# Kernel tuning notes

Hardware: AMD Instinct MI355X
Metric: run time of the kernel (lower is better)

The kernel has to match this reference:

```python
import jax, jax.numpy as jnp
import numpy as np

D_IN = 4096
D_OUT = 4096
RANK = 16
ALPHA = 32
SCALE = ALPHA / RANK


def setup_inputs() -> dict:
    key = jax.random.key(0)
    k_x, k_w, k_b, k_a = jax.random.split(key, 4)
    x = jax.random.normal(k_x, (4, 2048, D_IN), dtype=jnp.float32)
    weight = jax.random.normal(k_w, (D_OUT, D_IN), dtype=jnp.float32) * (1.0 / np.sqrt(D_IN))
    bias = jax.random.normal(k_b, (D_OUT,), dtype=jnp.float32)
    lora_A = jax.random.normal(k_a, (RANK, D_IN), dtype=jnp.float32) * 0.01
    lora_B = jnp.zeros((D_OUT, RANK), dtype=jnp.float32)
    return {"x": x, "weight": weight, "bias": bias, "lora_A": lora_A, "lora_B": lora_B}


def reference(x, weight, bias, lora_A, lora_B):
    # base linear: y = x @ W^T + b   -> [B, S, D_OUT]
    orig_out = jnp.einsum("bsd,od->bso", x, weight) + bias
    # low-rank path: (x @ A^T) @ B^T * (alpha/rank)
    lora_out = jnp.einsum("bsr,or->bso", jnp.einsum("bsd,rd->bsr", x, lora_A), lora_B)
    return orig_out + lora_out * SCALE
```

## Files before the change

### kernel.cpp

```cpp
#include <hip/hip_runtime.h>
#include <stdint.h>

#define DIN   4096
#define DOUT  4096
#define RANK  16
#define MTOT  8192
#define LSCALE 2.0f

typedef unsigned short u16;
typedef __bf16 bf16x8 __attribute__((ext_vector_type(8)));
typedef float  f32x4  __attribute__((ext_vector_type(4)));
typedef u16    u16x8  __attribute__((ext_vector_type(8)));

__device__ __forceinline__ u16 f2bf(float f) {
    uint32_t u = __builtin_bit_cast(uint32_t, f);
    u = (u + 0x7FFFu + ((u >> 16) & 1u)) >> 16;
    return (u16)u;
}

__device__ __forceinline__ u16x8 pack8(f32x4 a, f32x4 b) {
    u16x8 o;
    o[0] = f2bf(a[0]); o[1] = f2bf(a[1]); o[2] = f2bf(a[2]); o[3] = f2bf(a[3]);
    o[4] = f2bf(b[0]); o[5] = f2bf(b[1]); o[6] = f2bf(b[2]); o[7] = f2bf(b[3]);
    return o;
}

#define GLDS16(g, l) __builtin_amdgcn_global_load_lds( \
    (const __attribute__((address_space(1))) void*)(g), \
    (__attribute__((address_space(3))) void*)(l), 16, 0, 0)

__global__ __launch_bounds__(256) void k_convert_x(const float* __restrict__ x,
                                                   u16* __restrict__ xb) {
    long i = ((long)blockIdx.x * 256 + threadIdx.x) * 8;
    f32x4 a = *(const f32x4*)(x + i);
    f32x4 b = *(const f32x4*)(x + i + 4);
    *(u16x8*)(xb + i) = pack8(a, b);
}

__global__ __launch_bounds__(256) void k_build_weff(const float* __restrict__ W,
                                                    const float* __restrict__ A,
                                                    const float* __restrict__ B,
                                                    u16* __restrict__ wb) {
    long t = (long)blockIdx.x * 256 + threadIdx.x;
    long i = t * 8;
    int o = (int)(i >> 12);
    int d = (int)(i & (DIN - 1));
    float sB[RANK];
#pragma unroll
    for (int r = 0; r < RANK; ++r) sB[r] = B[o * RANK + r] * LSCALE;
    f32x4 w0 = *(const f32x4*)(W + i);
    f32x4 w1 = *(const f32x4*)(W + i + 4);
#pragma unroll
    for (int r = 0; r < RANK; ++r) {
        f32x4 a0 = *(const f32x4*)(A + (long)r * DIN + d);
        f32x4 a1 = *(const f32x4*)(A + (long)r * DIN + d + 4);
        w0 += a0 * sB[r];
        w1 += a1 * sB[r];
    }
    *(u16x8*)(wb + i) = pack8(w0, w1);
}

#define BM 256
#define BN 256
#define BK 64
#define NT (DIN / BK)

#define MFMA16(d, a, b) d = __builtin_amdgcn_mfma_f32_16x16x32_bf16(a, b, d, 0, 0, 0)
#define ABAR()   asm volatile("s_barrier" ::: "memory")
#define GATE8()  asm volatile("s_waitcnt vmcnt(8)" ::: "memory")
#define GATE10() asm volatile("s_waitcnt vmcnt(10)" ::: "memory")
#define PRIO1() __builtin_amdgcn_s_setprio(1)
#define PRIO0() __builtin_amdgcn_s_setprio(0)

#define QUADK(mo, no, AF, BF) \
    _Pragma("unroll") \
    for (int kk = 0; kk < 2; ++kk) { \
        _Pragma("unroll") \
        for (int m = 0; m < 4; ++m) { \
            _Pragma("unroll") \
            for (int n = 0; n < 2; ++n) { \
                MFMA16(acc[(mo)+m][(no)+n], AF[m][kk], BF[n][kk]); \
            } \
        } \
    }

#define READ_A4(DST, P, RB) \
    _Pragma("unroll") \
    for (int m = 0; m < 4; ++m) { \
        DST[m][0] = *(const bf16x8*)((P) + (RB) + m*1024 + go0); \
        DST[m][1] = *(const bf16x8*)((P) + (RB) + m*1024 + go1); \
    }
#define READ_B2(DST, P, RB) \
    _Pragma("unroll") \
    for (int n = 0; n < 2; ++n) { \
        DST[n][0] = *(const bf16x8*)((P) + (RB) + n*1024 + go0); \
        DST[n][1] = *(const bf16x8*)((P) + (RB) + n*1024 + go1); \
    }

__global__ __launch_bounds__(512, 2) void k_gemm_ws(const u16* __restrict__ xb,
                                                    const u16* __restrict__ wb,
                                                    const float* __restrict__ bias,
                                                    float* __restrict__ out) {
    constexpr int K = DIN, N = DOUT;
    __shared__ alignas(16) u16 lds[65536];

    const int nchunk = gridDim.x >> 3;
    const int bid = blockIdx.x;
    const int wg  = (bid & 7) * nchunk + (bid >> 3);
    const int bm  = (wg & 31) * BM;
    const int bn  = (wg >> 5) * BN;

    const int tid  = threadIdx.x;
    const int lane = tid & 63;
    const int wid  = tid >> 6;
    const int wr   = wid >> 2;
    const int wc   = wid & 3;
    const int lrow = lane & 15;
    const int kgrp = lane >> 4;

    const int srow = tid >> 3;
    const int sgl  = (tid & 7) ^ (srow & 7);
    const u16* const aSrcB = xb + (long)(bm + srow) * K + sgl * 8;
    const u16* const bSrcB = wb + (long)(bn + srow) * K + sgl * 8;

#define STAGE_A(c, buf, kt) GLDS16(aSrcB + (long)(64*(c))*K + (kt)*BK, \
                                   lds + (buf)*16384 + (c)*4096 + tid*8)
#define STAGE_B(c, buf, kt) GLDS16(bSrcB + (long)(64*(c))*K + (kt)*BK, \
                                   lds + 32768 + (buf)*16384 + (c)*4096 + tid*8)

    const int go0 = (kgrp ^ (lrow & 7)) * 8;
    const int go1 = go0 ^ 32;
    const int arL = (wr*64 + lrow) * 64;
    const int arH = arL + 128*64;
    const int brL = (wc*32 + lrow) * 64;
    const int brH = brL + 128*64;

    const u16* const pA0 = lds;
    const u16* const pA1 = lds + 16384;
    const u16* const pB0 = lds + 32768;
    const u16* const pB1 = lds + 49152;

    f32x4 acc[8][4];
#pragma unroll
    for (int m = 0; m < 8; ++m)
#pragma unroll
        for (int n = 0; n < 4; ++n) acc[m][n] = (f32x4){0.f, 0.f, 0.f, 0.f};

    bf16x8 afL[4][2], afH[4][2], bfB[2][2], bfAe[2][2], bfAo[2][2];

    STAGE_A(0, 0, 0); STAGE_A(1, 0, 0);
    STAGE_B(0, 0, 0); STAGE_B(1, 0, 0);
    STAGE_B(2, 0, 0); STAGE_B(3, 0, 0);
    STAGE_A(2, 0, 0); STAGE_A(3, 0, 0);
    STAGE_A(0, 1, 1); STAGE_A(1, 1, 1);
    STAGE_B(0, 1, 1); STAGE_B(1, 1, 1);
    STAGE_B(2, 1, 1); STAGE_B(3, 1, 1);
    GATE10();
    ABAR();
    READ_A4(afL, pA0, arL);
    READ_B2(bfAe, pB0, brL);

    for (int it = 0; it < NT/2; ++it) {
        const int t   = 2*it;
        const int kt1 = t + 1;
        const int kt2 = (t + 2) & (NT - 1);
        const int kt3 = (t + 3) & (NT - 1);

        GATE8(); ABAR();
        STAGE_A(2, 1, kt1); STAGE_A(3, 1, kt1);
        READ_B2(bfB, pB0, brH);
        PRIO1(); QUADK(0, 0, afL, bfAe); PRIO0();

        GATE8(); ABAR();
        STAGE_A(0, 0, kt2); STAGE_A(1, 0, kt2);
        READ_A4(afH, pA0, arH);
        PRIO1(); QUADK(0, 2, afL, bfB); PRIO0();

        ABAR();
        STAGE_B(0, 0, kt2); STAGE_B(1, 0, kt2);
        STAGE_B(2, 0, kt2); STAGE_B(3, 0, kt2);
        PRIO1(); QUADK(4, 2, afH, bfB); PRIO0();

        GATE10(); ABAR();
        READ_A4(afL, pA1, arL);
        READ_B2(bfAo, pB1, brL);
        PRIO1(); QUADK(4, 0, afH, bfAe); PRIO0();

        GATE8(); ABAR();
        STAGE_A(2, 0, kt2); STAGE_A(3, 0, kt2);
        READ_B2(bfB, pB1, brH);
        PRIO1(); QUADK(0, 0, afL, bfAo); PRIO0();

        GATE8(); ABAR();
        STAGE_A(0, 1, kt3); STAGE_A(1, 1, kt3);
        READ_A4(afH, pA1, arH);
        PRIO1(); QUADK(0, 2, afL, bfB); PRIO0();

        ABAR();
        STAGE_B(0, 1, kt3); STAGE_B(1, 1, kt3);
        STAGE_B(2, 1, kt3); STAGE_B(3, 1, kt3);
        PRIO1(); QUADK(4, 2, afH, bfB); PRIO0();

        GATE10(); ABAR();
        READ_A4(afL, pA0, arL);
        READ_B2(bfAe, pB0, brL);
        PRIO1(); QUADK(4, 0, afH, bfAo); PRIO0();
    }
    asm volatile("s_waitcnt vmcnt(0)" ::: "memory");

    const int orow = bm + wr*64 + kgrp*4;
    const int ocol = bn + wc*32 + lrow;
#pragma unroll
    for (int n = 0; n < 4; ++n) {
        const int col = ocol + (n & 1)*16 + (n >> 1)*128;
        const float bj = bias[col];
#pragma unroll
        for (int m = 0; m < 8; ++m) {
            const int row = orow + (m & 3)*16 + (m >> 2)*128;
#pragma unroll
            for (int r = 0; r < 4; ++r)
                out[(long)(row + r) * N + col] = acc[m][n][r] + bj;
        }
    }
}

__global__ __launch_bounds__(64) void k_lora_T(const float* __restrict__ x,
                                               const float* __restrict__ A,
                                               float* __restrict__ T) {
    const int m = blockIdx.x;
    const int lane = threadIdx.x;
    const float* xr = x + (long)m * DIN;
    float acc[RANK];
#pragma unroll
    for (int r = 0; r < RANK; ++r) acc[r] = 0.f;
    for (int k = lane * 4; k < DIN; k += 64 * 4) {
        f32x4 xv = *(const f32x4*)(xr + k);
#pragma unroll
        for (int r = 0; r < RANK; ++r) {
            f32x4 av = *(const f32x4*)(A + (long)r * DIN + k);
            acc[r] += xv[0] * av[0] + xv[1] * av[1] + xv[2] * av[2] + xv[3] * av[3];
        }
    }
#pragma unroll
    for (int r = 0; r < RANK; ++r)
        for (int off = 32; off > 0; off >>= 1) acc[r] += __shfl_down(acc[r], off);
    if (lane == 0) {
#pragma unroll
        for (int r = 0; r < RANK; ++r) T[(long)m * RANK + r] = acc[r] * LSCALE;
    }
}

__global__ __launch_bounds__(256) void k_gemm_nows(const float* __restrict__ x,
                                                   const float* __restrict__ W,
                                                   const float* __restrict__ bias,
                                                   const float* __restrict__ T,
                                                   const float* __restrict__ lB,
                                                   float* __restrict__ out) {
    constexpr int FBM = 128, FBN = 128, FBK = 32, K = DIN, N = DOUT;
    __shared__ __align__(16) u16 As[FBM * FBK];
    __shared__ __align__(16) u16 Bs[FBN * FBK];

    const int tid = threadIdx.x;
    const int bm = blockIdx.y * FBM;
    const int bn = blockIdx.x * FBN;
    const int lane = tid & 63;
    const int wid  = tid >> 6;
    const int wr = wid >> 1, wc = wid & 1;
    const int lrow = lane & 15;
    const int kgrp = lane >> 4;

    const int c0 = tid, c1 = tid + 256;
    const float* aS0 = x + (long)(bm + (c0 >> 2)) * K + (c0 & 3) * 8;
    const float* aS1 = x + (long)(bm + (c1 >> 2)) * K + (c1 & 3) * 8;
    const float* bS0 = W + (long)(bn + (c0 >> 2)) * K + (c0 & 3) * 8;
    const float* bS1 = W + (long)(bn + (c1 >> 2)) * K + (c1 & 3) * 8;
    u16* aD0 = As + c0 * 8;  u16* aD1 = As + c1 * 8;
    u16* bD0 = Bs + c0 * 8;  u16* bD1 = Bs + c1 * 8;

    const u16* aR = As + (wr * 64 + lrow) * FBK + kgrp * 8;
    const u16* bR = Bs + (wc * 64 + lrow) * FBK + kgrp * 8;

    f32x4 acc[4][4];
#pragma unroll
    for (int i = 0; i < 4; ++i)
#pragma unroll
        for (int j = 0; j < 4; ++j) acc[i][j] = (f32x4){0.f, 0.f, 0.f, 0.f};

    for (int k0 = 0; k0 < K; k0 += FBK) {
        f32x4 a00 = *(const f32x4*)aS0, a01 = *(const f32x4*)(aS0 + 4);
        f32x4 a10 = *(const f32x4*)aS1, a11 = *(const f32x4*)(aS1 + 4);
        f32x4 b00 = *(const f32x4*)bS0, b01 = *(const f32x4*)(bS0 + 4);
        f32x4 b10 = *(const f32x4*)bS1, b11 = *(const f32x4*)(bS1 + 4);
        aS0 += FBK; aS1 += FBK; bS0 += FBK; bS1 += FBK;
        if (k0) __syncthreads();
        *(u16x8*)aD0 = pack8(a00, a01);
        *(u16x8*)aD1 = pack8(a10, a11);
        *(u16x8*)bD0 = pack8(b00, b01);
        *(u16x8*)bD1 = pack8(b10, b11);
        __syncthreads();

        bf16x8 af[4], bf[4];
#pragma unroll
        for (int i = 0; i < 4; ++i) af[i] = *(const bf16x8*)(aR + i * 16 * FBK);
#pragma unroll
        for (int j = 0; j < 4; ++j) bf[j] = *(const bf16x8*)(bR + j * 16 * FBK);
#pragma unroll
        for (int i = 0; i < 4; ++i)
#pragma unroll
            for (int j = 0; j < 4; ++j)
                acc[i][j] = __builtin_amdgcn_mfma_f32_16x16x32_bf16(af[i], bf[j], acc[i][j], 0, 0, 0);
    }

#pragma unroll
    for (int j = 0; j < 4; ++j) {
        const int col = bn + wc * 64 + j * 16 + lrow;
        const float bj = bias[col];
        float bl[RANK];
#pragma unroll
        for (int q = 0; q < RANK; ++q) bl[q] = lB[(long)col * RANK + q];
#pragma unroll
        for (int i = 0; i < 4; ++i) {
            const int row0 = bm + wr * 64 + i * 16 + kgrp * 4;
#pragma unroll
            for (int r = 0; r < 4; ++r) {
                const int row = row0 + r;
                const float* Trow = T + (long)row * RANK;
                float s = bj;
#pragma unroll
                for (int q = 0; q < RANK; ++q) s += Trow[q] * bl[q];
                out[(long)row * N + col] = acc[i][j][r] + s;
            }
        }
    }
}

extern "C" void kernel_launch(void* const* d_in, const int* in_sizes, int n_in,
                              void* d_out, int out_size, void* d_ws, size_t ws_size,
                              hipStream_t stream) {
    const float* x    = (const float*)d_in[0];
    const float* W    = (const float*)d_in[1];
    const float* bias = (const float*)d_in[2];
    const float* lA   = (const float*)d_in[3];
    const float* lB   = (const float*)d_in[4];
    float* out = (float*)d_out;

    const size_t xb_bytes = (size_t)MTOT * DIN * sizeof(u16);
    const size_t wb_bytes = (size_t)DOUT * DIN * sizeof(u16);

    if (ws_size >= xb_bytes + wb_bytes) {
        u16* xb = (u16*)d_ws;
        u16* wb = (u16*)((char*)d_ws + xb_bytes);
        k_convert_x <<<(int)((long)MTOT * DIN / 8 / 256), 256, 0, stream>>>(x, xb);
        k_build_weff<<<(int)((long)DOUT * DIN / 8 / 256), 256, 0, stream>>>(W, lA, lB, wb);
        k_gemm_ws   <<<(MTOT / BM) * (DOUT / BN), 512, 0, stream>>>(xb, wb, bias, out);
    } else {
        float* T = (float*)d_ws;
        k_lora_T   <<<MTOT, 64, 0, stream>>>(x, lA, T);
        k_gemm_nows<<<dim3(DOUT / 128, MTOT / 128), 256, 0, stream>>>(x, W, bias, T, lB, out);
    }
}
```

Before: 332.2 us.

## Restructure GEMM main loop into single-tile four-phase pipeline with contiguous warp tiles

```diff
diff --git a/kernel.cpp b/kernel.cpp
--- a/kernel.cpp
+++ b/kernel.cpp
@@ -67,10 +67,11 @@
 
 #define MFMA16(d, a, b) d = __builtin_amdgcn_mfma_f32_16x16x32_bf16(a, b, d, 0, 0, 0)
 #define ABAR()   asm volatile("s_barrier" ::: "memory")
-#define GATE8()  asm volatile("s_waitcnt vmcnt(8)" ::: "memory")
-#define GATE10() asm volatile("s_waitcnt vmcnt(10)" ::: "memory")
-#define PRIO1() __builtin_amdgcn_s_setprio(1)
-#define PRIO0() __builtin_amdgcn_s_setprio(0)
+#define LGKM0()  asm volatile("s_waitcnt lgkmcnt(0)" ::: "memory")
+#define GATE4()  asm volatile("s_waitcnt vmcnt(4)" ::: "memory")
+#define SBAR0()  __builtin_amdgcn_sched_barrier(0)
+#define PRIO1()  __builtin_amdgcn_s_setprio(1)
+#define PRIO0()  __builtin_amdgcn_s_setprio(0)
 
 #define QUADK(mo, no, AF, BF) \
     _Pragma("unroll") \
@@ -84,19 +85,6 @@
         } \
     }
 
-#define READ_A4(DST, P, RB) \
-    _Pragma("unroll") \
-    for (int m = 0; m < 4; ++m) { \
-        DST[m][0] = *(const bf16x8*)((P) + (RB) + m*1024 + go0); \
-        DST[m][1] = *(const bf16x8*)((P) + (RB) + m*1024 + go1); \
-    }
-#define READ_B2(DST, P, RB) \
-    _Pragma("unroll") \
-    for (int n = 0; n < 2; ++n) { \
-        DST[n][0] = *(const bf16x8*)((P) + (RB) + n*1024 + go0); \
-        DST[n][1] = *(const bf16x8*)((P) + (RB) + n*1024 + go1); \
-    }
-
 __global__ __launch_bounds__(512, 2) void k_gemm_ws(const u16* __restrict__ xb,
                                                     const u16* __restrict__ wb,
                                                     const float* __restrict__ bias,
@@ -130,15 +118,8 @@
 
     const int go0 = (kgrp ^ (lrow & 7)) * 8;
     const int go1 = go0 ^ 32;
-    const int arL = (wr*64 + lrow) * 64;
-    const int arH = arL + 128*64;
-    const int brL = (wc*32 + lrow) * 64;
-    const int brH = brL + 128*64;
-
-    const u16* const pA0 = lds;
-    const u16* const pA1 = lds + 16384;
-    const u16* const pB0 = lds + 32768;
-    const u16* const pB1 = lds + 49152;
+    const int arow = (wr*128 + lrow) * 64;
+    const int brow = (wc*64  + lrow) * 64;
 
     f32x4 acc[8][4];
 #pragma unroll
@@ -146,77 +127,84 @@
 #pragma unroll
         for (int n = 0; n < 4; ++n) acc[m][n] = (f32x4){0.f, 0.f, 0.f, 0.f};
 
-    bf16x8 afL[4][2], afH[4][2], bfB[2][2], bfAe[2][2], bfAo[2][2];
+    bf16x8 af[4][2], bfLo[2][2], bfHi[2][2];
 
     STAGE_A(0, 0, 0); STAGE_A(1, 0, 0);
+    STAGE_A(2, 0, 0); STAGE_A(3, 0, 0);
     STAGE_B(0, 0, 0); STAGE_B(1, 0, 0);
     STAGE_B(2, 0, 0); STAGE_B(3, 0, 0);
-    STAGE_A(2, 0, 0); STAGE_A(3, 0, 0);
-    STAGE_A(0, 1, 1); STAGE_A(1, 1, 1);
     STAGE_B(0, 1, 1); STAGE_B(1, 1, 1);
     STAGE_B(2, 1, 1); STAGE_B(3, 1, 1);
-    GATE10();
-    ABAR();
-    READ_A4(afL, pA0, arL);
-    READ_B2(bfAe, pB0, brL);
-
-    for (int it = 0; it < NT/2; ++it) {
-        const int t   = 2*it;
-        const int kt1 = t + 1;
+    GATE4();
+    __syncthreads();
+
+    for (int t = 0; t < NT; ++t) {
+        const int cur = t & 1, nxt = cur ^ 1;
+        const int kt1 = (t + 1) & (NT - 1);
         const int kt2 = (t + 2) & (NT - 1);
-        const int kt3 = (t + 3) & (NT - 1);
-
-        GATE8(); ABAR();
-        STAGE_A(2, 1, kt1); STAGE_A(3, 1, kt1);
-        READ_B2(bfB, pB0, brH);
-        PRIO1(); QUADK(0, 0, afL, bfAe); PRIO0();
-
-        GATE8(); ABAR();
-        STAGE_A(0, 0, kt2); STAGE_A(1, 0, kt2);
-        READ_A4(afH, pA0, arH);
-        PRIO1(); QUADK(0, 2, afL, bfB); PRIO0();
-
-        ABAR();
-        STAGE_B(0, 0, kt2); STAGE_B(1, 0, kt2);
-        STAGE_B(2, 0, kt2); STAGE_B(3, 0, kt2);
-        PRIO1(); QUADK(4, 2, afH, bfB); PRIO0();
-
-        GATE10(); ABAR();
-        READ_A4(afL, pA1, arL);
-        READ_B2(bfAo, pB1, brL);
-        PRIO1(); QUADK(4, 0, afH, bfAe); PRIO0();
-
-        GATE8(); ABAR();
-        STAGE_A(2, 0, kt2); STAGE_A(3, 0, kt2);
-        READ_B2(bfB, pB1, brH);
-        PRIO1(); QUADK(0, 0, afL, bfAo); PRIO0();
-
-        GATE8(); ABAR();
-        STAGE_A(0, 1, kt3); STAGE_A(1, 1, kt3);
-        READ_A4(afH, pA1, arH);
-        PRIO1(); QUADK(0, 2, afL, bfB); PRIO0();
-
-        ABAR();
-        STAGE_B(0, 1, kt3); STAGE_B(1, 1, kt3);
-        STAGE_B(2, 1, kt3); STAGE_B(3, 1, kt3);
-        PRIO1(); QUADK(4, 2, afH, bfB); PRIO0();
-
-        GATE10(); ABAR();
-        READ_A4(afL, pA0, arL);
-        READ_B2(bfAe, pB0, brL);
-        PRIO1(); QUADK(4, 0, afH, bfAo); PRIO0();
+        const u16* const cA = lds + cur * 16384;
+        const u16* const cB = lds + 32768 + cur * 16384;
+
+#pragma unroll
+        for (int mf = 0; mf < 4; ++mf) {
+            const u16* b = cA + arow + mf * 1024;
+            af[mf][0] = *(const bf16x8*)(b + go0);
+            af[mf][1] = *(const bf16x8*)(b + go1);
+        }
+#pragma unroll
+        for (int nf = 0; nf < 2; ++nf) {
+            const u16* b = cB + brow + nf * 1024;
+            bfLo[nf][0] = *(const bf16x8*)(b + go0);
+            bfLo[nf][1] = *(const bf16x8*)(b + go1);
+        }
+        STAGE_A(0, nxt, kt1); STAGE_A(1, nxt, kt1);
+        ABAR();
+        LGKM0(); SBAR0();
+        PRIO1(); QUADK(0, 0, af, bfLo); PRIO0(); SBAR0();
+        ABAR();
+
+#pragma unroll
+        for (int nf = 0; nf < 2; ++nf) {
+            const u16* b = cB + brow + (nf + 2) * 1024;
+            bfHi[nf][0] = *(const bf16x8*)(b + go0);
+            bfHi[nf][1] = *(const bf16x8*)(b + go1);
+        }
+        STAGE_A(2, nxt, kt1); STAGE_A(3, nxt, kt1);
+        ABAR();
+        LGKM0(); SBAR0();
+        PRIO1(); QUADK(0, 2, af, bfHi); PRIO0(); SBAR0();
+        ABAR();
+
+#pragma unroll
+        for (int mf = 0; mf < 4; ++mf) {
+            const u16* b = cA + arow + (mf + 4) * 1024;
+            af[mf][0] = *(const bf16x8*)(b + go0);
+            af[mf][1] = *(const bf16x8*)(b + go1);
+        }
+        STAGE_B(0, cur, kt2); STAGE_B(1, cur, kt2);
+        ABAR();
+        LGKM0(); SBAR0();
+        PRIO1(); QUADK(4, 0, af, bfLo); PRIO0(); SBAR0();
+        ABAR();
+
+        STAGE_B(2, cur, kt2); STAGE_B(3, cur, kt2);
+        GATE4();
+        ABAR();
+        SBAR0();
+        PRIO1(); QUADK(4, 2, af, bfHi); PRIO0(); SBAR0();
+        ABAR();
     }
     asm volatile("s_waitcnt vmcnt(0)" ::: "memory");
 
-    const int orow = bm + wr*64 + kgrp*4;
-    const int ocol = bn + wc*32 + lrow;
+    const int orow = bm + wr*128 + kgrp*4;
+    const int ocol = bn + wc*64 + lrow;
 #pragma unroll
     for (int n = 0; n < 4; ++n) {
-        const int col = ocol + (n & 1)*16 + (n >> 1)*128;
+        const int col = ocol + n*16;
         const float bj = bias[col];
 #pragma unroll
         for (int m = 0; m < 8; ++m) {
-            const int row = orow + (m & 3)*16 + (m >> 2)*128;
+            const int row = orow + m*16;
 #pragma unroll
             for (int r = 0; r < 4; ++r)
                 out[(long)(row + r) * N + col] = acc[m][n][r] + bj;
```

Measured after the change: 332.8 us. No clear change (+0.2%).
